# Performance work log

Hardware: AMD Instinct MI355X
Metric: run time of the kernel (lower is better)

## Reference

```python
import jax, jax.numpy as jnp
import numpy as np

BLOCK_SIZE = 64
NUM_STEPS = 3
# pad_type='post', init_type='ones', attention_mask=None


def setup_inputs() -> dict:
    key = jax.random.key(0)
    k1, k2, k3 = jax.random.split(key, 3)
    B, H, S, D = 4, 16, 4096, 64
    return {
        "query": jax.random.normal(k1, (B, H, S, D), dtype=jnp.float32),
        "key": jax.random.normal(k2, (B, H, S, D), dtype=jnp.float32),
        "value": jax.random.normal(k3, (B, H, S, D), dtype=jnp.float32),
    }


def _soba_monarch(query, key, value):
    B, H, S, D = query.shape
    bs = BLOCK_SIZE
    nb = -(-S // bs)                 # ceil(S / bs)
    pad = nb * bs - S                # post padding amount
    q = query / (D ** 0.5)

    pad_cfg = ((0, 0), (0, 0), (0, pad), (0, 0))
    Qb = jnp.pad(q, pad_cfg).reshape(B, H, nb, bs, D)      # (l j) v -> l j v
    Kb = jnp.pad(key, pad_cfg).reshape(B, H, nb, bs, D)    # (k i) v -> k i v

    # validity of positions in the padded sequence (post-pad)
    pos_valid = (jnp.arange(nb * bs) < S).reshape(nb, bs)  # [block, within]
    # left factor shape (..., j, l, k): rows of the flattened (l j) axis
    left_mask = jnp.broadcast_to(pos_valid.T[:, :, None], (bs, nb, nb))      # j l k
    # right factor shape (..., k, j, i): columns of the flattened (k i) axis
    right_mask = jnp.broadcast_to(pos_valid[:, None, :], (nb, bs, bs))       # k j i

    NEG = jnp.finfo(q.dtype).min
    # init_type = 'ones'
    left = jnp.broadcast_to(
        jnp.where(left_mask, 1.0 / nb, 0.0), (B, H, bs, nb, nb)
    ).astype(q.dtype)

    for _ in range(NUM_STEPS):
        # beta[k,j,i] = sum_{l,v} left[j,l,k] Q[l,j,v] K[k,i,v]
        beta = jnp.einsum('bhjlk,bhljv,bhkiv->bhkji', left, Qb, Kb, optimize=True)
        tau = jnp.swapaxes(jnp.sum(left, axis=-2), -1, -2)[..., None]        # bhkj1
        tau_zero = jnp.isclose(tau, 0.0)
        tau_safe = jnp.where(tau_zero, 1.0, tau)
        logits_r = jnp.where(right_mask & ~tau_zero, beta / tau_safe, NEG)
        right = jax.nn.softmax(logits_r, axis=-1)
        right = jnp.where(right_mask, right, 0.0)

        # alpha[j,1,k] = sum_i right[k,j,i] log right[k,j,i]  (xlogy)
        r_safe = jnp.where(right > 0, right, 1.0)
        alpha = jnp.sum(right * jnp.log(r_safe), axis=-1)                    # bhkj
        alpha = jnp.swapaxes(alpha, -1, -2)[..., None, :]                    # bhj1k

        beta2 = jnp.einsum('bhkji,bhljv,bhkiv->bhjlk', right, Qb, Kb, optimize=True)
        left = jax.nn.softmax(jnp.where(left_mask, beta2 - alpha, NEG), axis=-1)
        left = jnp.where(left_mask, left, 0.0)

    # multiply: z = L (R V)
    Vb = jnp.pad(value, pad_cfg).reshape(B, H, nb, bs, D)                    # k i v
    Y = jnp.einsum('bhkji,bhkiv->bhkjv', right, Vb)
    Z = jnp.einsum('bhjlk,bhkjv->bhljv', left, Y)
    z = Z.reshape(B, H, nb * bs, D)
    return z[..., :S, :]


def reference(query, key, value):
    return _soba_monarch(query, key, value)
```

## Files before the change

kernel.cpp:

```cpp
#include <hip/hip_runtime.h>


namespace {

typedef __attribute__((ext_vector_type(8))) short short8v;
typedef __attribute__((ext_vector_type(4))) float f32x4;

constexpr int HEADS = 64;
constexpr size_t HEADQ = 262144;
constexpr size_t MATF  = (size_t)HEADS * 262144;

#define MFMA(ACC, A, B) ACC = __builtin_amdgcn_mfma_f32_16x16x32_bf16(A, B, ACC, 0, 0, 0)
#define LD8(arr, row, g8) (*(const short8v*)((arr) + (row) * 72 + (g8) * 8))

__device__ __forceinline__ void bfsplit(float x, ushort& h, ushort& l) {
    uint u = __float_as_uint(x);
    uint hi = (u + 0x7FFFu + ((u >> 16) & 1u)) & 0xFFFF0000u;
    h = (ushort)(hi >> 16);
    l = (ushort)(__float_as_uint(x - __uint_as_float(hi)) >> 16);
}

struct Frag16 { short8v h0, h1, l0, l1; };

__device__ __forceinline__ Frag16 split_load(const float* __restrict__ p, float s) {
    Frag16 f;
    #pragma unroll
    for (int q = 0; q < 4; ++q) {
        float4 a = *(const float4*)(p + 4 * q);
        float v[4] = {a.x * s, a.y * s, a.z * s, a.w * s};
        #pragma unroll
        for (int e = 0; e < 4; ++e) {
            ushort hh, ll; bfsplit(v[e], hh, ll);
            const int i = 4 * q + e;
            if (i < 8) { f.h0[i] = (short)hh; f.l0[i] = (short)ll; }
            else       { f.h1[i - 8] = (short)hh; f.l1[i - 8] = (short)ll; }
        }
    }
    return f;
}
__device__ __forceinline__ void store_rows(ushort* H, ushort* L, int r, int c0,
                                           const Frag16& f) {
    *(short8v*)(H + r * 72 + c0)     = f.h0;
    *(short8v*)(H + r * 72 + c0 + 8) = f.h1;
    *(short8v*)(L + r * 72 + c0)     = f.l0;
    *(short8v*)(L + r * 72 + c0 + 8) = f.l1;
}
__device__ __forceinline__ void scatter_tr(ushort* H, ushort* L, int r, int c0,
                                           const Frag16& f) {
    #pragma unroll
    for (int e = 0; e < 8; ++e) {
        H[(c0 + e) * 72 + r] = (ushort)f.h0[e];
        L[(c0 + e) * 72 + r] = (ushort)f.l0[e];
    }
    #pragma unroll
    for (int e = 0; e < 8; ++e) {
        H[(c0 + 8 + e) * 72 + r] = (ushort)f.h1[e];
        L[(c0 + 8 + e) * 72 + r] = (ushort)f.l1[e];
    }
}

__device__ __forceinline__ void flush_f32(const float* OS, float* g, int tid) {
    #pragma unroll
    for (int q = 0; q < 4; ++q) {
        const int off = tid * 4 + q * 1024;
        float4 v = *(const float4*)(OS + (off >> 6) * 68 + (off & 63));
        *(float4*)(g + off) = v;
    }
}

__device__ __forceinline__ void mmstep(const ushort* AH, const ushort* AL,
                                       const ushort* BH, const ushort* BL,
                                       int w, int lo4, int hi4, f32x4 acc[4]) {
    #pragma unroll
    for (int ks = 0; ks < 2; ++ks) {
        short8v ah = LD8(AH, 16 * w + lo4, hi4 + 4 * ks);
        short8v al = LD8(AL, 16 * w + lo4, hi4 + 4 * ks);
        #pragma unroll
        for (int t = 0; t < 4; ++t) {
            short8v bh = LD8(BH, 16 * t + lo4, hi4 + 4 * ks);
            short8v bl = LD8(BL, 16 * t + lo4, hi4 + 4 * ks);
            MFMA(acc[t], ah, bh); MFMA(acc[t], ah, bl); MFMA(acc[t], al, bh);
        }
    }
}
__device__ __forceinline__ void mmstep_swap(const ushort* AH, const ushort* AL,
                                            const ushort* BH, const ushort* BL,
                                            int w, int lo4, int hi4, f32x4 acc[4]) {
    #pragma unroll
    for (int ks = 0; ks < 2; ++ks) {
        short8v bh = LD8(AH, 16 * w + lo4, hi4 + 4 * ks);
        short8v bl = LD8(AL, 16 * w + lo4, hi4 + 4 * ks);
        #pragma unroll
        for (int m = 0; m < 4; ++m) {
            short8v ah = LD8(BH, 16 * m + lo4, hi4 + 4 * ks);
            short8v al = LD8(BL, 16 * m + lo4, hi4 + 4 * ks);
            MFMA(acc[m], ah, bh); MFMA(acc[m], ah, bl); MFMA(acc[m], al, bh);
        }
    }
}

__device__ __forceinline__ float max16(const float* x) {
    float a = fmaxf(fmaxf(x[0], x[1]), fmaxf(x[2], x[3]));
    float b = fmaxf(fmaxf(x[4], x[5]), fmaxf(x[6], x[7]));
    float c = fmaxf(fmaxf(x[8], x[9]), fmaxf(x[10], x[11]));
    float d = fmaxf(fmaxf(x[12], x[13]), fmaxf(x[14], x[15]));
    return fmaxf(fmaxf(a, b), fmaxf(c, d));
}

__global__ __launch_bounds__(256) void kmean_kernel(const float* __restrict__ Q,
                                                    float* __restrict__ M) {
    const int wg = blockIdx.x;
    const int h  = wg >> 4;
    const int j  = ((wg & 15) << 2) + (threadIdx.x >> 6);
    const int v  = threadIdx.x & 63;
    const float* base = Q + (size_t)h * HEADQ + (size_t)j * 64 + v;
    float acc = 0.f;
    #pragma unroll
    for (int l = 0; l < 64; ++l) acc += base[(size_t)l * 4096];
    M[((size_t)h * 64 + j) * 64 + v] = acc * (1.0f / 512.0f);
}

template<int FIRST, int LAST>
__global__ __launch_bounds__(256, 4) void bc_kernel(
    const float* __restrict__ Gsrc,
    const float* __restrict__ Kmat,
    const float* __restrict__ Vmat,
    const float* __restrict__ tauIn,
    float* __restrict__ HmOut,
    float* __restrict__ alphaOut,
    float* __restrict__ Yout)
{
    __shared__ __align__(16) ushort SM[18432];
    ushort* Ah = SM;          ushort* Al = SM + 4608;
    ushort* Bh = SM + 9216;   ushort* Bl = SM + 13824;
    float* OSA = (float*)SM;
    float* OSB = (float*)(SM + 9216);

    const int wg = blockIdx.x, h = wg >> 6, k = wg & 63;
    const int tid = threadIdx.x, r = tid & 63, c0 = (tid >> 6) << 4;
    const int w = tid >> 6, lo4 = tid & 15, hi4 = (tid >> 4) & 3;

    {
        const float* gp = FIRST ? Gsrc + ((size_t)h * 64 + r) * 64 + c0
                                : Gsrc + ((size_t)h * 64 + r) * 4096 + (size_t)k * 64 + c0;
        store_rows(Ah, Al, r, c0, split_load(gp, 1.f));
    }
    Frag16 fk = split_load(Kmat + (size_t)h * HEADQ + (size_t)k * 4096 + r * 64 + c0, 1.f);
    store_rows(Bh, Bl, r, c0, fk);
    Frag16 fv;
    if (LAST)
        fv = split_load(Vmat + (size_t)h * HEADQ + (size_t)k * 4096 + r * 64 + c0, 1.f);
    float tv = 1.f;
    if (!FIRST) tv = tauIn[((size_t)h * 64 + k) * 64 + 16 * w + lo4];
    __syncthreads();

    f32x4 acc[4] = {};
    mmstep_swap(Ah, Al, Bh, Bl, w, lo4, hi4, acc);
    __syncthreads();

    {
        const int j = 16 * w + lo4;
        const bool tz = !(tv > 1e-8f);
        const float tvi = tz ? 1.f : 1.f / tv;
        float x[16];
        #pragma unroll
        for (int m = 0; m < 4; ++m)
            #pragma unroll
            for (int rg = 0; rg < 4; ++rg) x[4 * m + rg] = acc[m][rg] * tvi;
        float mx = max16(x);
        mx = fmaxf(mx, __shfl_xor(mx, 16));
        mx = fmaxf(mx, __shfl_xor(mx, 32));
        float ex[16], s = 0.f, p = 0.f;
        #pragma unroll
        for (int e = 0; e < 16; ++e) {
            ex[e] = __expf(x[e] - mx);
            s += ex[e];
            p = fmaf(ex[e], x[e], p);
        }
        s += __shfl_xor(s, 16);
        s += __shfl_xor(s, 32);
        p += __shfl_xor(p, 16);
        p += __shfl_xor(p, 32);
        const float inv = 1.f / s;
        const float ap = tz ? -4.1588830834f
                            : fmaf(p, inv, -mx - __logf(s));
        #pragma unroll
        for (int m = 0; m < 4; ++m) {
            #pragma unroll
            for (int rg = 0; rg < 4; ++rg) {
                const float rv = tz ? (1.f / 64.f) : ex[4 * m + rg] * inv;
                ushort hh, ll; bfsplit(rv, hh, ll);
                const int i = 16 * m + 4 * hi4 + rg;
                Ah[j * 72 + i] = hh;
                Al[j * 72 + i] = ll;
            }
        }
        if (hi4 == 0) alphaOut[((size_t)h * 64 + j) * 64 + k] = ap;
    }
    scatter_tr(Bh, Bl, r, c0, fk);
    __syncthreads();

    f32x4 acc2[4] = {};
    mmstep(Ah, Al, Bh, Bl, w, lo4, hi4, acc2);
    const size_t ob = ((size_t)h * 64 + k) * 4096;
    if (!LAST) {
        __syncthreads();
        #pragma unroll
        for (int rr = 0; rr < 4; ++rr) {
            const int j = 16 * w + 4 * hi4 + rr;
            #pragma unroll
            for (int t = 0; t < 4; ++t)
                OSB[j * 68 + 16 * t + lo4] = acc2[t][rr];
        }
        __syncthreads();
        flush_f32(OSB, HmOut + ob, tid);
    } else {
        __syncthreads();
        scatter_tr(Bh, Bl, r, c0, fv);
        __syncthreads();
        f32x4 acc3[4] = {};
        mmstep(Ah, Al, Bh, Bl, w, lo4, hi4, acc3);
        __syncthreads();
        #pragma unroll
        for (int rr = 0; rr < 4; ++rr) {
            const int j = 16 * w + 4 * hi4 + rr;
            #pragma unroll
            for (int t = 0; t < 4; ++t) {
                OSA[j * 68 + 16 * t + lo4] = acc2[t][rr];
                OSB[j * 68 + 16 * t + lo4] = acc3[t][rr];
            }
        }
        __syncthreads();
        flush_f32(OSA, HmOut + ob, tid);
        flush_f32(OSB, Yout + ob, tid);
    }
}

template<int LAST>
__global__ __launch_bounds__(256, 4) void da_kernel(
    const float* __restrict__ Q,
    const float* __restrict__ HmIn,
    const float* __restrict__ alphaIn,
    const float* __restrict__ Yin,
    float* __restrict__ Gout,
    float* __restrict__ tauOut,
    float* __restrict__ Zout)
{
    __shared__ __align__(16) ushort SM[18432];
    ushort* Ah = SM;          ushort* Al = SM + 4608;
    ushort* Bh = SM + 9216;   ushort* Bl = SM + 13824;
    float* OSB = (float*)(SM + 9216);

    const int wg = blockIdx.x, h = wg >> 6, j = wg & 63;
    const int tid = threadIdx.x, r = tid & 63, c0 = (tid >> 6) << 4;
    const int w = tid >> 6, lo4 = tid & 15, hi4 = (tid >> 4) & 3;

    Frag16 fq = split_load(Q + (size_t)h * HEADQ + (size_t)r * 4096 + (size_t)j * 64 + c0,
                           0.125f);
    store_rows(Ah, Al, r, c0, fq);
    {
        store_rows(Bh, Bl, r, c0,
                   split_load(HmIn + ((size_t)h * 64 + r) * 4096 + (size_t)j * 64 + c0, 1.f));
    }
    Frag16 fy;
    if (LAST)
        fy = split_load(Yin + ((size_t)h * 64 + r) * 4096 + (size_t)j * 64 + c0, 1.f);
    float av[16];
    {
        const float* ap0 = alphaIn + ((size_t)h * 64 + j) * 64 + 4 * hi4;
        #pragma unroll
        for (int m = 0; m < 4; ++m)
            #pragma unroll
            for (int rg = 0; rg < 4; ++rg) av[4 * m + rg] = ap0[16 * m + rg];
    }
    __syncthreads();

    f32x4 acc[4] = {};
    mmstep_swap(Ah, Al, Bh, Bl, w, lo4, hi4, acc);
    __syncthreads();

    {
        const int l = 16 * w + lo4;
        float x[16];
        #pragma unroll
        for (int m = 0; m < 4; ++m)
            #pragma unroll
            for (int rg = 0; rg < 4; ++rg) x[4 * m + rg] = acc[m][rg] - av[4 * m + rg];
        float mx = max16(x);
        mx = fmaxf(mx, __shfl_xor(mx, 16));
        mx = fmaxf(mx, __shfl_xor(mx, 32));
        #pragma unroll
        for (int e = 0; e < 16; ++e) x[e] = __expf(x[e] - mx);
        float s = 0.f;
        #pragma unroll
        for (int e = 0; e < 16; ++e) s += x[e];
        s += __shfl_xor(s, 16);
        s += __shfl_xor(s, 32);
        const float inv = 1.f / s;
        #pragma unroll
        for (int m = 0; m < 4; ++m) {
            #pragma unroll
            for (int rg = 0; rg < 4; ++rg) {
                const float lv = x[4 * m + rg] * inv;
                ushort hh, ll; bfsplit(lv, hh, ll);
                const int kk = 16 * m + 4 * hi4 + rg;
                if (!LAST) { Bh[kk * 72 + l] = hh; Bl[kk * 72 + l] = ll; }
                else       { Bh[l * 72 + kk] = hh; Bl[l * 72 + kk] = ll; }
            }
        }
    }
    if (!LAST) scatter_tr(Ah, Al, r, c0, fq);
    else       scatter_tr(Ah, Al, r, c0, fy);
    __syncthreads();

    if (!LAST) {
        f32x4 acc2[4] = {};
        f32x4 tacc = {};
        short8v onesb;
        #pragma unroll
        for (int e2 = 0; e2 < 8; ++e2) onesb[e2] = (lo4 == 0) ? (short)0x3F80 : (short)0;
        #pragma unroll
        for (int ks = 0; ks < 2; ++ks) {
            short8v ah = LD8(Bh, 16 * w + lo4, hi4 + 4 * ks);
            short8v al = LD8(Bl, 16 * w + lo4, hi4 + 4 * ks);
            MFMA(tacc, ah, onesb); MFMA(tacc, al, onesb);
            #pragma unroll
            for (int t = 0; t < 4; ++t) {
                short8v bh = LD8(Ah, 16 * t + lo4, hi4 + 4 * ks);
                short8v bl = LD8(Al, 16 * t + lo4, hi4 + 4 * ks);
                MFMA(acc2[t], ah, bh); MFMA(acc2[t], ah, bl); MFMA(acc2[t], al, bh);
            }
        }
        __syncthreads();
        #pragma unroll
        for (int rr = 0; rr < 4; ++rr) {
            const int kq = 16 * w + 4 * hi4 + rr;
            if (lo4 == 0) tauOut[((size_t)h * 64 + kq) * 64 + j] = tacc[rr];
            #pragma unroll
            for (int t = 0; t < 4; ++t)
                OSB[kq * 68 + 16 * t + lo4] = acc2[t][rr];
        }
        __syncthreads();
        flush_f32(OSB, Gout + ((size_t)h * 64 + j) * 4096, tid);
    } else {
        f32x4 acc2[4] = {};
        #pragma unroll
        for (int ks = 0; ks < 2; ++ks) {
            short8v ah = LD8(Bh, 16 * w + lo4, hi4 + 4 * ks);
            short8v al = LD8(Bl, 16 * w + lo4, hi4 + 4 * ks);
            #pragma unroll
            for (int t = 0; t < 4; ++t) {
                short8v bh = LD8(Ah, 16 * t + lo4, hi4 + 4 * ks);
                short8v bl = LD8(Al, 16 * t + lo4, hi4 + 4 * ks);
                MFMA(acc2[t], ah, bh); MFMA(acc2[t], ah, bl); MFMA(acc2[t], al, bh);
            }
        }
        __syncthreads();
        #pragma unroll
        for (int rr = 0; rr < 4; ++rr) {
            const int l = 16 * w + 4 * hi4 + rr;
            #pragma unroll
            for (int t = 0; t < 4; ++t) OSB[l * 68 + 16 * t + lo4] = acc2[t][rr];
        }
        __syncthreads();
        #pragma unroll
        for (int q = 0; q < 4; ++q) {
            const int l = (tid >> 4) + 16 * q;
            const int v4 = (tid & 15) * 4;
            float4 vv = *(const float4*)(OSB + l * 68 + v4);
            *(float4*)(Zout + (size_t)h * HEADQ + (size_t)l * 4096 + (size_t)j * 64 + v4) = vv;
        }
    }
}

}

extern "C" void kernel_launch(void* const* d_in, const int* in_sizes, int n_in,
                              void* d_out, int out_size, void* d_ws, size_t ws_size,
                              hipStream_t stream) {
    const float* Q = (const float*)d_in[0];
    const float* K = (const float*)d_in[1];
    const float* V = (const float*)d_in[2];
    float* out = (float*)d_out;

    char* ws = (char*)d_ws;
    const size_t MB = 1024 * 1024;
    float* G   = (float*)(ws);
    float* Hm  = (float*)(ws + 64 * MB);
    float* M   = (float*)(ws + 128 * MB);
    float* al  = (float*)(ws + 129 * MB);
    float* tau = (float*)(ws + 130 * MB);

    const bool bigws = ws_size >= (size_t)195 * MB;
    float* Ybuf = bigws ? (float*)(ws + 131 * MB) : out;
    float* Zdst = bigws ? out : G;

    dim3 blk(256), grid(HEADS * 64);

    kmean_kernel<<<dim3(1024), blk, 0, stream>>>(Q, M);
    bc_kernel<1, 0><<<grid, blk, 0, stream>>>(M, K, nullptr, nullptr, Hm, al, nullptr);
    da_kernel<0>   <<<grid, blk, 0, stream>>>(Q, Hm, al, nullptr, G, tau, nullptr);
    bc_kernel<0, 0><<<grid, blk, 0, stream>>>(G, K, nullptr, tau, Hm, al, nullptr);
    da_kernel<0>   <<<grid, blk, 0, stream>>>(Q, Hm, al, nullptr, G, tau, nullptr);
    bc_kernel<0, 1><<<grid, blk, 0, stream>>>(G, K, V, tau, Hm, al, Ybuf);
    da_kernel<1>   <<<grid, blk, 0, stream>>>(Q, Hm, al, Ybuf, nullptr, nullptr, Zdst);
    if (!bigws)
        hipMemcpyAsync(d_out, Zdst, MATF * sizeof(float), hipMemcpyDeviceToDevice, stream);
}
```

Baseline: 302.3 us.

## Store intermediates as pre-split swizzled bf16 hi/lo and load via direct-to-LDS

```diff
diff --git a/kernel.cpp b/kernel.cpp
--- a/kernel.cpp
+++ b/kernel.cpp
@@ -11,7 +11,19 @@
 constexpr size_t MATF  = (size_t)HEADS * 262144;
 
 #define MFMA(ACC, A, B) ACC = __builtin_amdgcn_mfma_f32_16x16x32_bf16(A, B, ACC, 0, 0, 0)
-#define LD8(arr, row, g8) (*(const short8v*)((arr) + (row) * 72 + (g8) * 8))
+
+__device__ __forceinline__ void gload16(const ushort* g, ushort* l) {
+    __builtin_amdgcn_global_load_lds(
+        (const __attribute__((address_space(1))) void*)g,
+        (__attribute__((address_space(3))) void*)l, 16, 0, 0);
+}
+
+__device__ __forceinline__ int swz(int row, int col) {
+    return row * 64 + (((col >> 3) ^ (row & 7)) << 3) + (col & 7);
+}
+__device__ __forceinline__ short8v ldx(const ushort* a, int row, int chunk) {
+    return *(const short8v*)(a + row * 64 + ((chunk ^ (row & 7)) << 3));
+}
 
 __device__ __forceinline__ void bfsplit(float x, ushort& h, ushort& l) {
     uint u = __float_as_uint(x);
@@ -40,32 +52,29 @@
 }
 __device__ __forceinline__ void store_rows(ushort* H, ushort* L, int r, int c0,
                                            const Frag16& f) {
-    *(short8v*)(H + r * 72 + c0)     = f.h0;
-    *(short8v*)(H + r * 72 + c0 + 8) = f.h1;
-    *(short8v*)(L + r * 72 + c0)     = f.l0;
-    *(short8v*)(L + r * 72 + c0 + 8) = f.l1;
+    const int ch = c0 >> 3;
+    const int o0 = r * 64 + ((ch ^ (r & 7)) << 3);
+    const int o1 = r * 64 + (((ch + 1) ^ (r & 7)) << 3);
+    *(short8v*)(H + o0) = f.h0; *(short8v*)(H + o1) = f.h1;
+    *(short8v*)(L + o0) = f.l0; *(short8v*)(L + o1) = f.l1;
 }
 __device__ __forceinline__ void scatter_tr(ushort* H, ushort* L, int r, int c0,
                                            const Frag16& f) {
     #pragma unroll
     for (int e = 0; e < 8; ++e) {
-        H[(c0 + e) * 72 + r] = (ushort)f.h0[e];
-        L[(c0 + e) * 72 + r] = (ushort)f.l0[e];
+        H[swz(c0 + e, r)] = (ushort)f.h0[e];
+        L[swz(c0 + e, r)] = (ushort)f.l0[e];
     }
     #pragma unroll
     for (int e = 0; e < 8; ++e) {
-        H[(c0 + 8 + e) * 72 + r] = (ushort)f.h1[e];
-        L[(c0 + 8 + e) * 72 + r] = (ushort)f.l1[e];
-    }
-}
-
-__device__ __forceinline__ void flush_f32(const float* OS, float* g, int tid) {
-    #pragma unroll
-    for (int q = 0; q < 4; ++q) {
-        const int off = tid * 4 + q * 1024;
-        float4 v = *(const float4*)(OS + (off >> 6) * 68 + (off & 63));
-        *(float4*)(g + off) = v;
-    }
+        H[swz(c0 + 8 + e, r)] = (ushort)f.h1[e];
+        L[swz(c0 + 8 + e, r)] = (ushort)f.l1[e];
+    }
+}
+
+__device__ __forceinline__ void flush8k(const ushort* S, ushort* g, int tid) {
+    *(short8v*)(g + tid * 8)        = *(const short8v*)(S + tid * 8);
+    *(short8v*)(g + 2048 + tid * 8) = *(const short8v*)(S + 2048 + tid * 8);
 }
 
 __device__ __forceinline__ void mmstep(const ushort* AH, const ushort* AL,
@@ -73,12 +82,12 @@
                                        int w, int lo4, int hi4, f32x4 acc[4]) {
     #pragma unroll
     for (int ks = 0; ks < 2; ++ks) {
-        short8v ah = LD8(AH, 16 * w + lo4, hi4 + 4 * ks);
-        short8v al = LD8(AL, 16 * w + lo4, hi4 + 4 * ks);
+        short8v ah = ldx(AH, 16 * w + lo4, hi4 + 4 * ks);
+        short8v al = ldx(AL, 16 * w + lo4, hi4 + 4 * ks);
         #pragma unroll
         for (int t = 0; t < 4; ++t) {
-            short8v bh = LD8(BH, 16 * t + lo4, hi4 + 4 * ks);
-            short8v bl = LD8(BL, 16 * t + lo4, hi4 + 4 * ks);
+            short8v bh = ldx(BH, 16 * t + lo4, hi4 + 4 * ks);
+            short8v bl = ldx(BL, 16 * t + lo4, hi4 + 4 * ks);
             MFMA(acc[t], ah, bh); MFMA(acc[t], ah, bl); MFMA(acc[t], al, bh);
         }
     }
@@ -88,12 +97,12 @@
                                             int w, int lo4, int hi4, f32x4 acc[4]) {
     #pragma unroll
     for (int ks = 0; ks < 2; ++ks) {
-        short8v bh = LD8(AH, 16 * w + lo4, hi4 + 4 * ks);
-        short8v bl = LD8(AL, 16 * w + lo4, hi4 + 4 * ks);
+        short8v bh = ldx(AH, 16 * w + lo4, hi4 + 4 * ks);
+        short8v bl = ldx(AL, 16 * w + lo4, hi4 + 4 * ks);
         #pragma unroll
         for (int m = 0; m < 4; ++m) {
-            short8v ah = LD8(BH, 16 * m + lo4, hi4 + 4 * ks);
-            short8v al = LD8(BL, 16 * m + lo4, hi4 + 4 * ks);
+            short8v ah = ldx(BH, 16 * m + lo4, hi4 + 4 * ks);
+            short8v al = ldx(BL, 16 * m + lo4, hi4 + 4 * ks);
             MFMA(acc[m], ah, bh); MFMA(acc[m], ah, bl); MFMA(acc[m], al, bh);
         }
     }
@@ -108,7 +117,8 @@
 }
 
 __global__ __launch_bounds__(256) void kmean_kernel(const float* __restrict__ Q,
-                                                    float* __restrict__ M) {
+                                                    ushort* __restrict__ Mh,
+                                                    ushort* __restrict__ Ml) {
     const int wg = blockIdx.x;
     const int h  = wg >> 4;
     const int j  = ((wg & 15) << 2) + (threadIdx.x >> 6);
@@ -117,33 +127,47 @@
     float acc = 0.f;
     #pragma unroll
     for (int l = 0; l < 64; ++l) acc += base[(size_t)l * 4096];
-    M[((size_t)h * 64 + j) * 64 + v] = acc * (1.0f / 512.0f);
+    ushort hh, ll; bfsplit(acc * (1.0f / 512.0f), hh, ll);
+    const int idx = swz(j, v);
+    Mh[(size_t)h * 4096 + idx] = hh;
+    Ml[(size_t)h * 4096 + idx] = ll;
 }
 
 template<int FIRST, int LAST>
 __global__ __launch_bounds__(256, 4) void bc_kernel(
-    const float* __restrict__ Gsrc,
-    const float* __restrict__ Kmat,
-    const float* __restrict__ Vmat,
-    const float* __restrict__ tauIn,
-    float* __restrict__ HmOut,
-    float* __restrict__ alphaOut,
-    float* __restrict__ Yout)
+    const ushort* __restrict__ Gh,
+    const ushort* __restrict__ Gl,
+    const float*  __restrict__ Kmat,
+    const float*  __restrict__ Vmat,
+    const float*  __restrict__ tauIn,
+    ushort* __restrict__ Hmh,
+    ushort* __restrict__ Hml,
+    float*  __restrict__ alphaOut,
+    ushort* __restrict__ Yh,
+    ushort* __restrict__ Yl)
 {
-    __shared__ __align__(16) ushort SM[18432];
-    ushort* Ah = SM;          ushort* Al = SM + 4608;
-    ushort* Bh = SM + 9216;   ushort* Bl = SM + 13824;
-    float* OSA = (float*)SM;
-    float* OSB = (float*)(SM + 9216);
+    __shared__ __align__(16) ushort SM[16384];
+    ushort* Ah = SM;          ushort* Al = SM + 4096;
+    ushort* Bh = SM + 8192;   ushort* Bl = SM + 12288;
 
     const int wg = blockIdx.x, h = wg >> 6, k = wg & 63;
     const int tid = threadIdx.x, r = tid & 63, c0 = (tid >> 6) << 4;
     const int w = tid >> 6, lo4 = tid & 15, hi4 = (tid >> 4) & 3;
 
-    {
-        const float* gp = FIRST ? Gsrc + ((size_t)h * 64 + r) * 64 + c0
-                                : Gsrc + ((size_t)h * 64 + r) * 4096 + (size_t)k * 64 + c0;
-        store_rows(Ah, Al, r, c0, split_load(gp, 1.f));
+    #pragma unroll
+    for (int a = 0; a < 2; ++a) {
+        const int o = a * 4096 + tid * 16;
+        size_t src;
+        if (FIRST) {
+            src = (size_t)h * 4096 + (size_t)(o >> 1);
+        } else {
+            const int row = o >> 7, cd = (o >> 4) & 7;
+            const int cu = cd ^ (row & 7);
+            src = ((size_t)h * 64 + row) * 4096 + (size_t)k * 64
+                + (size_t)((cu ^ (k & 7)) << 3);
+        }
+        gload16(Gh + src, (ushort*)((char*)Ah + o));
+        gload16(Gl + src, (ushort*)((char*)Al + o));
     }
     Frag16 fk = split_load(Kmat + (size_t)h * HEADQ + (size_t)k * 4096 + r * 64 + c0, 1.f);
     store_rows(Bh, Bl, r, c0, fk);
@@ -190,9 +214,8 @@
             for (int rg = 0; rg < 4; ++rg) {
                 const float rv = tz ? (1.f / 64.f) : ex[4 * m + rg] * inv;
                 ushort hh, ll; bfsplit(rv, hh, ll);
-                const int i = 16 * m + 4 * hi4 + rg;
-                Ah[j * 72 + i] = hh;
-                Al[j * 72 + i] = ll;
+                const int idx = swz(j, 16 * m + 4 * hi4 + rg);
+                Ah[idx] = hh; Al[idx] = ll;
             }
         }
         if (hi4 == 0) alphaOut[((size_t)h * 64 + j) * 64 + k] = ap;
@@ -209,11 +232,15 @@
         for (int rr = 0; rr < 4; ++rr) {
             const int j = 16 * w + 4 * hi4 + rr;
             #pragma unroll
-            for (int t = 0; t < 4; ++t)
-                OSB[j * 68 + 16 * t + lo4] = acc2[t][rr];
-        }
-        __syncthreads();
-        flush_f32(OSB, HmOut + ob, tid);
+            for (int t = 0; t < 4; ++t) {
+                ushort hh, ll; bfsplit(acc2[t][rr], hh, ll);
+                const int idx = swz(j, 16 * t + lo4);
+                Bh[idx] = hh; Bl[idx] = ll;
+            }
+        }
+        __syncthreads();
+        flush8k(Bh, Hmh + ob, tid);
+        flush8k(Bl, Hml + ob, tid);
     } else {
         __syncthreads();
         scatter_tr(Bh, Bl, r, c0, fv);
@@ -226,45 +253,67 @@
             const int j = 16 * w + 4 * hi4 + rr;
             #pragma unroll
             for (int t = 0; t < 4; ++t) {
-                OSA[j * 68 + 16 * t + lo4] = acc2[t][rr];
-                OSB[j * 68 + 16 * t + lo4] = acc3[t][rr];
-            }
-        }
-        __syncthreads();
-        flush_f32(OSA, HmOut + ob, tid);
-        flush_f32(OSB, Yout + ob, tid);
+                const int idx = swz(j, 16 * t + lo4);
+                ushort hh, ll;
+                bfsplit(acc2[t][rr], hh, ll);
+                Ah[idx] = hh; Al[idx] = ll;
+                bfsplit(acc3[t][rr], hh, ll);
+                Bh[idx] = hh; Bl[idx] = ll;
+            }
+        }
+        __syncthreads();
+        flush8k(Ah, Hmh + ob, tid);
+        flush8k(Al, Hml + ob, tid);
+        flush8k(Bh, Yh + ob, tid);
+        flush8k(Bl, Yl + ob, tid);
     }
 }
 
 template<int LAST>
 __global__ __launch_bounds__(256, 4) void da_kernel(
-    const float* __restrict__ Q,
-    const float* __restrict__ HmIn,
-    const float* __restrict__ alphaIn,
-    const float* __restrict__ Yin,
-    float* __restrict__ Gout,
-    float* __restrict__ tauOut,
-    float* __restrict__ Zout)
+    const float*  __restrict__ Q,
+    const ushort* __restrict__ Hmh,
+    const ushort* __restrict__ Hml,
+    const float*  __restrict__ alphaIn,
+    const ushort* __restrict__ Yh,
+    const ushort* __restrict__ Yl,
+    ushort* __restrict__ Goh,
+    ushort* __restrict__ Gol,
+    float*  __restrict__ tauOut,
+    float*  __restrict__ Zout)
 {
-    __shared__ __align__(16) ushort SM[18432];
-    ushort* Ah = SM;          ushort* Al = SM + 4608;
-    ushort* Bh = SM + 9216;   ushort* Bl = SM + 13824;
-    float* OSB = (float*)(SM + 9216);
+    __shared__ __align__(16) ushort SM[16384];
+    ushort* Ah = SM;          ushort* Al = SM + 4096;
+    ushort* Bh = SM + 8192;   ushort* Bl = SM + 12288;
+    float* OSZ = (float*)(SM + 8192);
 
     const int wg = blockIdx.x, h = wg >> 6, j = wg & 63;
     const int tid = threadIdx.x, r = tid & 63, c0 = (tid >> 6) << 4;
     const int w = tid >> 6, lo4 = tid & 15, hi4 = (tid >> 4) & 3;
 
+    #pragma unroll
+    for (int a = 0; a < 2; ++a) {
+        const int o = a * 4096 + tid * 16;
+        const int kd = o >> 7, cd = (o >> 4) & 7;
+        const int cu = cd ^ (kd & 7);
+        const size_t src = ((size_t)h * 64 + kd) * 4096 + (size_t)j * 64
+                         + (size_t)((cu ^ (j & 7)) << 3);
+        gload16(Hmh + src, (ushort*)((char*)Bh + o));
+        gload16(Hml + src, (ushort*)((char*)Bl + o));
+    }
     Frag16 fq = split_load(Q + (size_t)h * HEADQ + (size_t)r * 4096 + (size_t)j * 64 + c0,
                            0.125f);
     store_rows(Ah, Al, r, c0, fq);
-    {
-        store_rows(Bh, Bl, r, c0,
-                   split_load(HmIn + ((size_t)h * 64 + r) * 4096 + (size_t)j * 64 + c0, 1.f));
-    }
     Frag16 fy;
-    if (LAST)
-        fy = split_load(Yin + ((size_t)h * 64 + r) * 4096 + (size_t)j * 64 + c0, 1.f);
+    if (LAST) {
+        const size_t yb = ((size_t)h * 64 + r) * 4096 + (size_t)j * 64;
+        const int ch = c0 >> 3;
+        const int sA = ((ch ^ (j & 7)) << 3), sB = (((ch + 1) ^ (j & 7)) << 3);
+        fy.h0 = *(const short8v*)(Yh + yb + sA);
+        fy.h1 = *(const short8v*)(Yh + yb + sB);
+        fy.l0 = *(const short8v*)(Yl + yb + sA);
+        fy.l1 = *(const short8v*)(Yl + yb + sB);
+    }
     float av[16];
     {
         const float* ap0 = alphaIn + ((size_t)h * 64 + j) * 64 + 4 * hi4;
@@ -304,8 +353,8 @@
                 const float lv = x[4 * m + rg] * inv;
                 ushort hh, ll; bfsplit(lv, hh, ll);
                 const int kk = 16 * m + 4 * hi4 + rg;
-                if (!LAST) { Bh[kk * 72 + l] = hh; Bl[kk * 72 + l] = ll; }
-                else       { Bh[l * 72 + kk] = hh; Bl[l * 72 + kk] = ll; }
+                const int idx = LAST ? swz(l, kk) : swz(kk, l);
+                Bh[idx] = hh; Bl[idx] = ll;
             }
         }
     }
@@ -321,13 +370,13 @@
         for (int e2 = 0; e2 < 8; ++e2) onesb[e2] = (lo4 == 0) ? (short)0x3F80 : (short)0;
         #pragma unroll
         for (int ks = 0; ks < 2; ++ks) {
-            short8v ah = LD8(Bh, 16 * w + lo4, hi4 + 4 * ks);
-            short8v al = LD8(Bl, 16 * w + lo4, hi4 + 4 * ks);
+            short8v ah = ldx(Bh, 16 * w + lo4, hi4 + 4 * ks);
+            short8v al = ldx(Bl, 16 * w + lo4, hi4 + 4 * ks);
             MFMA(tacc, ah, onesb); MFMA(tacc, al, onesb);
             #pragma unroll
             for (int t = 0; t < 4; ++t) {
-                short8v bh = LD8(Ah, 16 * t + lo4, hi4 + 4 * ks);
-                short8v bl = LD8(Al, 16 * t + lo4, hi4 + 4 * ks);
+                short8v bh = ldx(Ah, 16 * t + lo4, hi4 + 4 * ks);
+                short8v bl = ldx(Al, 16 * t + lo4, hi4 + 4 * ks);
                 MFMA(acc2[t], ah, bh); MFMA(acc2[t], ah, bl); MFMA(acc2[t], al, bh);
             }
         }
@@ -337,21 +386,26 @@
             const int kq = 16 * w + 4 * hi4 + rr;
             if (lo4 == 0) tauOut[((size_t)h * 64 + kq) * 64 + j] = tacc[rr];
             #pragma unroll
-            for (int t = 0; t < 4; ++t)
-                OSB[kq * 68 + 16 * t + lo4] = acc2[t][rr];
-        }
-        __syncthreads();
-        flush_f32(OSB, Gout + ((size_t)h * 64 + j) * 4096, tid);
+            for (int t = 0; t < 4; ++t) {
+                ushort hh, ll; bfsplit(acc2[t][rr], hh, ll);
+                const int idx = swz(kq, 16 * t + lo4);
+                Bh[idx] = hh; Bl[idx] = ll;
+            }
+        }
+        __syncthreads();
+        const size_t ob = ((size_t)h * 64 + j) * 4096;
+        flush8k(Bh, Goh + ob, tid);
+        flush8k(Bl, Gol + ob, tid);
     } else {
         f32x4 acc2[4] = {};
         #pragma unroll
         for (int ks = 0; ks < 2; ++ks) {
-            short8v ah = LD8(Bh, 16 * w + lo4, hi4 + 4 * ks);
-            short8v al = LD8(Bl, 16 * w + lo4, hi4 + 4 * ks);
+            short8v ah = ldx(Bh, 16 * w + lo4, hi4 + 4 * ks);
+            short8v al = ldx(Bl, 16 * w + lo4, hi4 + 4 * ks);
             #pragma unroll
             for (int t = 0; t < 4; ++t) {
-                short8v bh = LD8(Ah, 16 * t + lo4, hi4 + 4 * ks);
-                short8v bl = LD8(Al, 16 * t + lo4, hi4 + 4 * ks);
+                short8v bh = ldx(Ah, 16 * t + lo4, hi4 + 4 * ks);
+                short8v bl = ldx(Al, 16 * t + lo4, hi4 + 4 * ks);
                 MFMA(acc2[t], ah, bh); MFMA(acc2[t], ah, bl); MFMA(acc2[t], al, bh);
             }
         }
@@ -360,15 +414,15 @@
         for (int rr = 0; rr < 4; ++rr) {
             const int l = 16 * w + 4 * hi4 + rr;
             #pragma unroll
-            for (int t = 0; t < 4; ++t) OSB[l * 68 + 16 * t + lo4] = acc2[t][rr];
+            for (int t = 0; t < 4; ++t) OSZ[l * 64 + 16 * t + lo4] = acc2[t][rr];
         }
         __syncthreads();
         #pragma unroll
         for (int q = 0; q < 4; ++q) {
-            const int l = (tid >> 4) + 16 * q;
+            const int lrow = (tid >> 4) + 16 * q;
             const int v4 = (tid & 15) * 4;
-            float4 vv = *(const float4*)(OSB + l * 68 + v4);
-            *(float4*)(Zout + (size_t)h * HEADQ + (size_t)l * 4096 + (size_t)j * 64 + v4) = vv;
+            float4 vv = *(const float4*)(OSZ + lrow * 64 + v4);
+            *(float4*)(Zout + (size_t)h * HEADQ + (size_t)lrow * 4096 + (size_t)j * 64 + v4) = vv;
         }
     }
 }
@@ -385,25 +439,35 @@
 
     char* ws = (char*)d_ws;
     const size_t MB = 1024 * 1024;
-    float* G   = (float*)(ws);
-    float* Hm  = (float*)(ws + 64 * MB);
-    float* M   = (float*)(ws + 128 * MB);
-    float* al  = (float*)(ws + 129 * MB);
-    float* tau = (float*)(ws + 130 * MB);
+    ushort* Gh  = (ushort*)(ws);
+    ushort* Gl  = (ushort*)(ws + 32 * MB);
+    ushort* Hmh = (ushort*)(ws + 64 * MB);
+    ushort* Hml = (ushort*)(ws + 96 * MB);
+    ushort* Mh  = (ushort*)(ws + 128 * MB);
+    ushort* Ml  = (ushort*)(ws + 128 * MB + 512 * 1024);
+    float*  al  = (float*)(ws + 129 * MB);
+    float*  tau = (float*)(ws + 130 * MB);
 
     const bool bigws = ws_size >= (size_t)195 * MB;
-    float* Ybuf = bigws ? (float*)(ws + 131 * MB) : out;
-    float* Zdst = bigws ? out : G;
+    ushort* Yh = bigws ? (ushort*)(ws + 131 * MB) : (ushort*)out;
+    ushort* Yl = bigws ? (ushort*)(ws + 163 * MB) : (ushort*)out + 16777216;
+    float*  Zdst = bigws ? out : (float*)ws;
 
     dim3 blk(256), grid(HEADS * 64);
 
-    kmean_kernel<<<dim3(1024), blk, 0, stream>>>(Q, M);
-    bc_kernel<1, 0><<<grid, blk, 0, stream>>>(M, K, nullptr, nullptr, Hm, al, nullptr);
-    da_kernel<0>   <<<grid, blk, 0, stream>>>(Q, Hm, al, nullptr, G, tau, nullptr);
-    bc_kernel<0, 0><<<grid, blk, 0, stream>>>(G, K, nullptr, tau, Hm, al, nullptr);
-    da_kernel<0>   <<<grid, blk, 0, stream>>>(Q, Hm, al, nullptr, G, tau, nullptr);
-    bc_kernel<0, 1><<<grid, blk, 0, stream>>>(G, K, V, tau, Hm, al, Ybuf);
-    da_kernel<1>   <<<grid, blk, 0, stream>>>(Q, Hm, al, Ybuf, nullptr, nullptr, Zdst);
+    kmean_kernel<<<dim3(1024), blk, 0, stream>>>(Q, Mh, Ml);
+    bc_kernel<1, 0><<<grid, blk, 0, stream>>>(Mh, Ml, K, nullptr, nullptr,
+                                              Hmh, Hml, al, nullptr, nullptr);
+    da_kernel<0>   <<<grid, blk, 0, stream>>>(Q, Hmh, Hml, al, nullptr, nullptr,
+                                              Gh, Gl, tau, nullptr);
+    bc_kernel<0, 0><<<grid, blk, 0, stream>>>(Gh, Gl, K, nullptr, tau,
+                                              Hmh, Hml, al, nullptr, nullptr);
+    da_kernel<0>   <<<grid, blk, 0, stream>>>(Q, Hmh, Hml, al, nullptr, nullptr,
+                                              Gh, Gl, tau, nullptr);
+    bc_kernel<0, 1><<<grid, blk, 0, stream>>>(Gh, Gl, K, V, tau,
+                                              Hmh, Hml, al, Yh, Yl);
+    da_kernel<1>   <<<grid, blk, 0, stream>>>(Q, Hmh, Hml, al, Yh, Yl,
+                                              nullptr, nullptr, nullptr, Zdst);
     if (!bigws)
         hipMemcpyAsync(d_out, Zdst, MATF * sizeof(float), hipMemcpyDeviceToDevice, stream);
 }
```

Result: no change. 300.5 us (-0.6%).
